# Kernel optimization log

Measured on AMD Instinct MI355X. Metric: run time of the kernel, lower is better.

Reference implementation:

```python
import jax, jax.numpy as jnp
import numpy as np

B, S = 2, 2048
HID, NH, NKV, HD = 4096, 32, 8, 128
THETA = 10000.0
WINDOW = 1024  # sliding window size


def setup_inputs() -> dict:
    key = jax.random.key(0)
    k1, k2, k3 = jax.random.split(key, 3)
    hidden_states = jax.random.normal(k1, (B, S, HID), jnp.float32)
    wqkv = jax.random.normal(k2, (HID, (NH + 2 * NKV) * HD), jnp.float32) * 0.02
    wo = jax.random.normal(k3, (NH * HD, HID), jnp.float32) * 0.02
    positions = jnp.arange(S, dtype=jnp.int32)
    return {"hidden_states": hidden_states, "wqkv": wqkv, "wo": wo, "positions": positions}


def _rope_neox(x, positions):
    # x: [B, S, h, HD]; GPT-NeoX style: rotate concatenated halves.
    half = HD // 2
    inv_freq = 1.0 / (THETA ** (jnp.arange(half, dtype=jnp.float32) / half))
    ang = positions.astype(jnp.float32)[:, None] * inv_freq  # [S, half]
    cos = jnp.cos(ang)[None, :, None, :]
    sin = jnp.sin(ang)[None, :, None, :]
    x1, x2 = jnp.split(x, 2, axis=-1)
    return jnp.concatenate([x1 * cos - x2 * sin, x2 * cos + x1 * sin], axis=-1)


def reference(hidden_states, wqkv, wo, positions):
    qkv = hidden_states @ wqkv  # [B, S, (NH+2*NKV)*HD]
    q, k, v = jnp.split(qkv, [NH * HD, NH * HD + NKV * HD], axis=-1)
    q = q.reshape(B, S, NH, HD)
    k = k.reshape(B, S, NKV, HD)
    v = v.reshape(B, S, NKV, HD)
    q = _rope_neox(q, positions)
    k = _rope_neox(k, positions)
    # GQA: each KV head serves NH // NKV query heads
    rep = NH // NKV
    k = jnp.repeat(k, rep, axis=2)  # [B, S, NH, HD]
    v = jnp.repeat(v, rep, axis=2)
    scale = HD ** -0.5
    scores = jnp.einsum('bqhd,bkhd->bhqk', q, k) * scale  # [B, NH, S, S]
    i = jnp.arange(S)[:, None]
    j = jnp.arange(S)[None, :]
    mask = (j <= i) & (i - j < WINDOW)  # causal + sliding window
    scores = jnp.where(mask[None, None], scores, jnp.float32(-1e30))
    probs = jax.nn.softmax(scores, axis=-1)
    attn = jnp.einsum('bhqk,bkhd->bqhd', probs, v).reshape(B, S, NH * HD)
    return attn @ wo  # [B, S, HID]
```

## Files before the change

kernel.cpp:

```cpp
#include <hip/hip_runtime.h>


typedef __attribute__((ext_vector_type(8))) short short8;
typedef __attribute__((ext_vector_type(4))) float f32x4;
typedef __attribute__((ext_vector_type(16))) float f32x16;
typedef __attribute__((ext_vector_type(4))) unsigned int u32x4;
typedef __attribute__((ext_vector_type(4))) unsigned short u16x4;

__device__ __forceinline__ unsigned short f2bf(float f) {
  unsigned int u = __builtin_bit_cast(unsigned int, f);
  u = u + 0x7fffu + ((u >> 16) & 1u);
  return (unsigned short)(u >> 16);
}
__device__ __forceinline__ float bf2f(unsigned short h) {
  unsigned int u = ((unsigned int)h) << 16;
  return __builtin_bit_cast(float, u);
}
__device__ __forceinline__ unsigned int cvtpk_bf16(float lo, float hi) {
  unsigned int r;
  asm("v_cvt_pk_bf16_f32 %0, %1, %2" : "=v"(r) : "v"(lo), "v"(hi));
  return r;
}

__device__ __forceinline__ void gload_lds16(const unsigned short* g, unsigned short* l) {
  __builtin_amdgcn_global_load_lds(
      (const __attribute__((address_space(1))) unsigned int*)g,
      (__attribute__((address_space(3))) unsigned int*)l, 16, 0, 0);
}

__device__ __forceinline__ void lds_barrier() {
  asm volatile("s_waitcnt lgkmcnt(0)" ::: "memory");
  __builtin_amdgcn_s_barrier();
}

#define MFMA16(A, B, C) __builtin_amdgcn_mfma_f32_16x16x32_bf16((A), (B), (C), 0, 0, 0)
#define MFMA32(A, B, C) __builtin_amdgcn_mfma_f32_32x32x16_bf16((A), (B), (C), 0, 0, 0)
#define BC8(x) __builtin_bit_cast(short8, (x))

__global__ __launch_bounds__(256) void cvt1(const float* __restrict__ hs,
                                            const float* __restrict__ wqkv,
                                            unsigned short* __restrict__ hsb,
                                            unsigned short* __restrict__ wT) {
  const int bid = blockIdx.x;
  if (bid < 24576) {
    __shared__ float t[32][33];
    const int c0 = (bid % 192) * 32, r0 = (bid / 192) * 32;
    const int tx = threadIdx.x & 31, ty = threadIdx.x >> 5;
#pragma unroll
    for (int i = 0; i < 4; ++i)
      t[ty + i * 8][tx] = wqkv[(size_t)(r0 + ty + i * 8) * 6144 + c0 + tx];
    __syncthreads();
#pragma unroll
    for (int i = 0; i < 4; ++i)
      wT[(size_t)(c0 + ty + i * 8) * 4096 + r0 + tx] = f2bf(t[tx][ty + i * 8]);
  } else {
    const int i = ((bid - 24576) * 256 + threadIdx.x) * 4;
    f32x4 v = *(const f32x4*)(hs + i);
    u16x4 o;
#pragma unroll
    for (int j = 0; j < 4; ++j) o[j] = f2bf(v[j]);
    *(u16x4*)(hsb + i) = o;
  }
}

__global__ __launch_bounds__(256) void rope_cvtwo(unsigned short* __restrict__ qkv,
                                                  const int* __restrict__ pos,
                                                  const float* __restrict__ wo,
                                                  unsigned short* __restrict__ wT) {
  const int bid = blockIdx.x;
  if (bid < 8192) {
    const int idx = bid * 256 + threadIdx.x;
    const int d = idx & 63;
    const int hh = (idx >> 6) & 7;
    const int tok = idx >> 9;
    const int s = tok & 2047;
    unsigned short* p = qkv + (size_t)tok * 6144 + 4096 + hh * 128 + d;
    const float x1 = bf2f(p[0]);
    const float x2 = bf2f(p[64]);
    const float inv = exp2f(-(float)d * 0.2076205059304601f);
    const float ang = (float)pos[s] * inv;
    const float c = cosf(ang), sn = sinf(ang);
    p[0]  = f2bf(x1 * c - x2 * sn);
    p[64] = f2bf(x2 * c + x1 * sn);
  } else {
    __shared__ float t[32][33];
    const int b2 = bid - 8192;
    const int c0 = (b2 % 128) * 32, r0 = (b2 / 128) * 32;
    const int tx = threadIdx.x & 31, ty = threadIdx.x >> 5;
#pragma unroll
    for (int i = 0; i < 4; ++i)
      t[ty + i * 8][tx] = wo[(size_t)(r0 + ty + i * 8) * 4096 + c0 + tx];
    __syncthreads();
#pragma unroll
    for (int i = 0; i < 4; ++i)
      wT[(size_t)(c0 + ty + i * 8) * 4096 + r0 + tx] = f2bf(t[tx][ty + i * 8]);
  }
}

template <int NIF, int OUTF32>
__global__ __launch_bounds__(512, 2) void gemm256(const unsigned short* __restrict__ A,
                                                  const unsigned short* __restrict__ BT,
                                                  void* __restrict__ Cout,
                                                  int M, int N, int K) {
  constexpr int BUFE = 16384 + NIF * 4096;
  constexpr int NR = NIF + 4;
  __shared__ __align__(16) unsigned short lds[2][BUFE];
  const int tid = threadIdx.x;
  const int lane = tid & 63;
  const int w = tid >> 6;
  const int wr = w >> 2;
  const int wc = w & 3;
  const int g = lane >> 4;
  const int l15 = lane & 15;

  const int nwg = gridDim.x;
  const int cpx = nwg >> 3;
  const int bid = blockIdx.x;
  const int swz = (bid & 7) * cpx + (bid >> 3);
  const int MT = M >> 8;
  const int m0 = (swz % MT) * 256;
  const int n0 = (swz / MT) * (NIF * 64);

  const int lrow = lane >> 3;
  const int lcol = ((lane & 7) ^ lrow) * 8;
  const unsigned short* Asrc = A + (size_t)(m0 + w * 8 + lrow) * K + lcol;
  const unsigned short* Bsrc = BT + (size_t)(n0 + w * 8 + lrow) * K + lcol;

  f32x4 acc[8][NIF] = {};

  auto stage = [&](int buf, int t, int r) {
    if (r < NIF) {
      const int rb = r * 64;
      gload_lds16(Bsrc + (size_t)rb * K + t * 64,
                  &lds[buf][16384 + (rb + w * 8) * 64]);
    } else {
      const int j = r - NIF;
      const int rb = (j & 1) * 128 + ((j >> 1) & 1) * 64;
      gload_lds16(Asrc + (size_t)rb * K + t * 64,
                  &lds[buf][(rb + w * 8) * 64]);
    }
  };
  auto rdA = [&](int buf, int mi, int ks) {
    const int row = wr * 128 + mi * 16 + l15;
    const int cb = (ks * 64 + g * 16) ^ ((l15 & 7) << 4);
    return *(const u32x4*)((const char*)&lds[buf][0] + row * 128 + cb);
  };
  auto rdB = [&](int buf, int ni, int ks) {
    const int row = wc * (NIF * 16) + ni * 16 + l15;
    const int cb = (ks * 64 + g * 16) ^ ((l15 & 7) << 4);
    return *(const u32x4*)((const char*)&lds[buf][0] + 32768 + row * 128 + cb);
  };

#pragma unroll
  for (int r = 0; r < NR; ++r) stage(0, 0, r);

  const int NT = K >> 6;
  for (int t = 0; t < NT; ++t) {
    const int cb_ = t & 1, nb_ = cb_ ^ 1;

    asm volatile("s_waitcnt vmcnt(0)" ::: "memory");
    __builtin_amdgcn_s_barrier();
    asm volatile("" ::: "memory");
    if (t + 1 < NT) {
#pragma unroll
      for (int r = 0; r < NR; ++r) stage(nb_, t + 1, r);
    }

    u32x4 bfr[NIF][2];
#pragma unroll
    for (int ni = 0; ni < NIF; ++ni) {
      bfr[ni][0] = rdB(cb_, ni, 0);
      bfr[ni][1] = rdB(cb_, ni, 1);
    }

    {
      u32x4 af[3][2];
#pragma unroll
      for (int mi = 0; mi < 3; ++mi) {
        af[mi][0] = rdA(cb_, mi, 0);
        af[mi][1] = rdA(cb_, mi, 1);
      }
      __builtin_amdgcn_s_setprio(1);
#pragma unroll
      for (int mi = 0; mi < 3; ++mi)
#pragma unroll
        for (int ni = 0; ni < NIF; ++ni) {
          acc[mi][ni] = MFMA16(BC8(af[mi][0]), BC8(bfr[ni][0]), acc[mi][ni]);
          acc[mi][ni] = MFMA16(BC8(af[mi][1]), BC8(bfr[ni][1]), acc[mi][ni]);
        }
      __builtin_amdgcn_s_setprio(0);
    }
    __builtin_amdgcn_s_barrier();
    {
      u32x4 af[3][2];
#pragma unroll
      for (int mi = 0; mi < 3; ++mi) {
        af[mi][0] = rdA(cb_, 3 + mi, 0);
        af[mi][1] = rdA(cb_, 3 + mi, 1);
      }
      __builtin_amdgcn_s_setprio(1);
#pragma unroll
      for (int mi = 0; mi < 3; ++mi)
#pragma unroll
        for (int ni = 0; ni < NIF; ++ni) {
          acc[3 + mi][ni] = MFMA16(BC8(af[mi][0]), BC8(bfr[ni][0]), acc[3 + mi][ni]);
          acc[3 + mi][ni] = MFMA16(BC8(af[mi][1]), BC8(bfr[ni][1]), acc[3 + mi][ni]);
        }
      __builtin_amdgcn_s_setprio(0);
    }
    __builtin_amdgcn_s_barrier();
    {
      u32x4 af[2][2];
#pragma unroll
      for (int mi = 0; mi < 2; ++mi) {
        af[mi][0] = rdA(cb_, 6 + mi, 0);
        af[mi][1] = rdA(cb_, 6 + mi, 1);
      }
      __builtin_amdgcn_s_setprio(1);
#pragma unroll
      for (int mi = 0; mi < 2; ++mi)
#pragma unroll
        for (int ni = 0; ni < NIF; ++ni) {
          acc[6 + mi][ni] = MFMA16(BC8(af[mi][0]), BC8(bfr[ni][0]), acc[6 + mi][ni]);
          acc[6 + mi][ni] = MFMA16(BC8(af[mi][1]), BC8(bfr[ni][1]), acc[6 + mi][ni]);
        }
      __builtin_amdgcn_s_setprio(0);
    }
  }

  const int crow0 = m0 + wr * 128;
  const int ccol0 = n0 + wc * (NIF * 16);
#pragma unroll
  for (int mi = 0; mi < 8; ++mi)
#pragma unroll
    for (int ni = 0; ni < NIF; ++ni)
#pragma unroll
      for (int r = 0; r < 4; ++r) {
        const size_t idx =
            (size_t)(crow0 + mi * 16 + g * 4 + r) * N + (ccol0 + ni * 16 + l15);
        if constexpr (OUTF32) ((float*)Cout)[idx] = acc[mi][ni][r];
        else ((unsigned short*)Cout)[idx] = f2bf(acc[mi][ni][r]);
      }
}

__global__ __launch_bounds__(512, 2) void attn_kernel(const unsigned short* __restrict__ qkv,
                                                      unsigned short* __restrict__ aout,
                                                      const int* __restrict__ pos) {
  __shared__ __align__(16) unsigned short smem[35840];

  const int tid = threadIdx.x;
  const int lane = tid & 63;
  const int w = tid >> 6;
  const int hi = lane >> 5;
  const int l31 = lane & 31;
  const int q0 = blockIdx.x * 256;
  const int h = blockIdx.y;
  const int b = blockIdx.z;
  const int kh = h >> 2;
  const size_t tokbase = (size_t)b * 2048;
  const int qw0 = q0 + w * 32;
  const int qg = qw0 + l31;

  short8 qf[8];
  {
    const unsigned short* qp = qkv + (tokbase + qg) * 6144 + h * 128;
#pragma unroll
    for (int ks8 = 0; ks8 < 8; ++ks8)
      qf[ks8] = BC8(*(const u32x4*)(qp + ks8 * 16 + hi * 8));
    const float fp = (float)pos[qg];
#pragma unroll
    for (int ks8 = 0; ks8 < 4; ++ks8)
#pragma unroll
      for (int j = 0; j < 8; ++j) {
        const int d = ks8 * 16 + hi * 8 + j;
        const float x1 = bf2f((unsigned short)qf[ks8][j]);
        const float x2 = bf2f((unsigned short)qf[ks8 + 4][j]);
        const float ang = fp * exp2f(-(float)d * 0.2076205059304601f);
        float c, sn;
        __sincosf(ang, &sn, &c);
        c *= 0.12751743f; sn *= 0.12751743f;
        qf[ks8][j]     = (short)f2bf(x1 * c - x2 * sn);
        qf[ks8 + 4][j] = (short)f2bf(x2 * c + x1 * sn);
      }
  }

  const int c0key = tid >> 4, c0col = tid & 15;
  const int c1key = (tid + 512) >> 4, c1col = tid & 15;

  u32x4 kreg[2], vreg[2];
  const unsigned short* kvK = qkv + tokbase * 6144 + 4096 + kh * 128;

  const int t0 = (q0 >= 1024 ? (q0 - 1023) >> 6 : 0);
  const int t1 = (q0 + 255) >> 6;

  {
    const unsigned short* kb = kvK + (size_t)(t0 * 64) * 6144;
    kreg[0] = *(const u32x4*)(kb + (size_t)c0key * 6144 + c0col * 8);
    kreg[1] = *(const u32x4*)(kb + (size_t)c1key * 6144 + c1col * 8);
    vreg[0] = *(const u32x4*)(kb + (size_t)c0key * 6144 + 1024 + c0col * 8);
    vreg[1] = *(const u32x4*)(kb + (size_t)c1key * 6144 + 1024 + c1col * 8);
  }

  float m_run = -1e30f, l_run = 0.0f;
  f32x16 o_acc[4] = {};

  for (int kt = t0; kt <= t1; ++kt) {
    const int cur = (kt - t0) & 1;
    unsigned short* kdst = &smem[(cur)*17920];
    unsigned short* vdst = kdst + 8704;

    if (kt == t0) {
      *(u32x4*)&kdst[c0key * 136 + c0col * 8] = kreg[0];
      *(u32x4*)&kdst[c1key * 136 + c1col * 8] = kreg[1];
#pragma unroll
      for (int e = 0; e < 8; ++e) {
        const int e0 = (e + c0col) & 7;
        const int e1 = (e + c1col) & 7;
        vdst[(c0col * 8 + e0) * 72 + c0key] =
            (unsigned short)(vreg[0][e0 >> 1] >> ((e0 & 1) * 16));
        vdst[(c1col * 8 + e1) * 72 + c1key] =
            (unsigned short)(vreg[1][e1 >> 1] >> ((e1 & 1) * 16));
      }
      if (kt < t1) {
        const unsigned short* kb = kvK + (size_t)((kt + 1) * 64) * 6144;
        kreg[0] = *(const u32x4*)(kb + (size_t)c0key * 6144 + c0col * 8);
        kreg[1] = *(const u32x4*)(kb + (size_t)c1key * 6144 + c1col * 8);
        vreg[0] = *(const u32x4*)(kb + (size_t)c0key * 6144 + 1024 + c0col * 8);
        vreg[1] = *(const u32x4*)(kb + (size_t)c1key * 6144 + 1024 + c1col * 8);
      }
      lds_barrier();
    }

    if (kt < t1) {
      unsigned short* kdn = &smem[(cur ^ 1) * 17920];
      unsigned short* vdn = kdn + 8704;
      *(u32x4*)&kdn[c0key * 136 + c0col * 8] = kreg[0];
      *(u32x4*)&kdn[c1key * 136 + c1col * 8] = kreg[1];
#pragma unroll
      for (int e = 0; e < 8; ++e) {
        const int e0 = (e + c0col) & 7;
        const int e1 = (e + c1col) & 7;
        vdn[(c0col * 8 + e0) * 72 + c0key] =
            (unsigned short)(vreg[0][e0 >> 1] >> ((e0 & 1) * 16));
        vdn[(c1col * 8 + e1) * 72 + c1key] =
            (unsigned short)(vreg[1][e1 >> 1] >> ((e1 & 1) * 16));
      }
      if (kt + 2 <= t1) {
        const unsigned short* kb = kvK + (size_t)((kt + 2) * 64) * 6144;
        kreg[0] = *(const u32x4*)(kb + (size_t)c0key * 6144 + c0col * 8);
        kreg[1] = *(const u32x4*)(kb + (size_t)c1key * 6144 + c1col * 8);
        vreg[0] = *(const u32x4*)(kb + (size_t)c0key * 6144 + 1024 + c0col * 8);
        vreg[1] = *(const u32x4*)(kb + (size_t)c1key * 6144 + 1024 + c1col * 8);
      }
    }

    const int ktb = kt * 64;
    if (ktb <= qw0 + 31 && ktb + 63 >= qw0 - 1023) {
      const unsigned short* kb = &smem[cur * 17920];
      const unsigned short* vb = kb + 8704;

      f32x16 s0 = {}, s1 = {};
      const int arow = l31 * 136 + hi * 8;
#pragma unroll
      for (int ks8 = 0; ks8 < 8; ++ks8) {
        u32x4 a0 = *(const u32x4*)&kb[arow + ks8 * 16];
        u32x4 a1 = *(const u32x4*)&kb[arow + 32 * 136 + ks8 * 16];
        s0 = MFMA32(BC8(a0), qf[ks8], s0);
        s1 = MFMA32(BC8(a1), qf[ks8], s1);
      }

      float pv[32];
      const bool need_mask = !(ktb + 63 <= qw0 && ktb >= qw0 - 992);
      if (need_mask) {
#pragma unroll
        for (int r = 0; r < 16; ++r) {
          const int key0 = ktb + ((r & 3) + 8 * (r >> 2) + 4 * hi);
          const int key1 = key0 + 32;
          pv[r]      = (key0 <= qg && qg - key0 < 1024) ? s0[r] : -1e30f;
          pv[16 + r] = (key1 <= qg && qg - key1 < 1024) ? s1[r] : -1e30f;
        }
      } else {
#pragma unroll
        for (int r = 0; r < 16; ++r) {
          pv[r] = s0[r];
          pv[16 + r] = s1[r];
        }
      }

      float mx[16];
#pragma unroll
      for (int i = 0; i < 16; ++i) mx[i] = fmaxf(pv[i], pv[i + 16]);
#pragma unroll
      for (int i = 0; i < 8; ++i) mx[i] = fmaxf(mx[i], mx[i + 8]);
#pragma unroll
      for (int i = 0; i < 4; ++i) mx[i] = fmaxf(mx[i], mx[i + 4]);
      float tm = fmaxf(fmaxf(mx[0], mx[1]), fmaxf(mx[2], mx[3]));
      tm = fmaxf(tm, __shfl_xor(tm, 32, 64));
      if (__any(tm > m_run + 11.5415603f)) {
        const float mn = fmaxf(fmaxf(m_run, tm), -1e20f);
        const float scl = exp2f(m_run - mn);
#pragma unroll
        for (int d = 0; d < 4; ++d) o_acc[d] *= scl;
        l_run *= scl;
        m_run = mn;
      }
#pragma unroll
      for (int i = 0; i < 32; ++i) pv[i] = exp2f(pv[i] - m_run);
      float sm[16];
#pragma unroll
      for (int i = 0; i < 16; ++i) sm[i] = pv[i] + pv[i + 16];
#pragma unroll
      for (int i = 0; i < 8; ++i) sm[i] = sm[i] + sm[i + 8];
#pragma unroll
      for (int i = 0; i < 4; ++i) sm[i] = sm[i] + sm[i + 4];
      float lsum = (sm[0] + sm[1]) + (sm[2] + sm[3]);
      l_run += lsum + __shfl_xor(lsum, 32, 64);

      u32x4 paf[4];
#pragma unroll
      for (int ks = 0; ks < 4; ++ks) {
        const int base = (ks >> 1) * 16 + (ks & 1) * 8;
        auto rA = __builtin_amdgcn_permlane32_swap(
            (int)cvtpk_bf16(pv[base + 0], pv[base + 1]),
            (int)cvtpk_bf16(pv[base + 4], pv[base + 5]), false, false);
        auto rB = __builtin_amdgcn_permlane32_swap(
            (int)cvtpk_bf16(pv[base + 2], pv[base + 3]),
            (int)cvtpk_bf16(pv[base + 6], pv[base + 7]), false, false);
        paf[ks][0] = (unsigned int)rA[0];
        paf[ks][1] = (unsigned int)rB[0];
        paf[ks][2] = (unsigned int)rA[1];
        paf[ks][3] = (unsigned int)rB[1];
      }

#pragma unroll
      for (int dblk = 0; dblk < 4; ++dblk) {
        const int vrow = (dblk * 32 + l31) * 72 + hi * 8;
#pragma unroll
        for (int ks = 0; ks < 4; ++ks) {
          u32x4 vf = *(const u32x4*)&vb[vrow + ks * 16];
          o_acc[dblk] = MFMA32(BC8(vf), BC8(paf[ks]), o_acc[dblk]);
        }
      }
    }

    lds_barrier();
  }

  const float rl = 1.0f / l_run;
  unsigned short* ob = &smem[w * 4352];
#pragma unroll
  for (int dblk = 0; dblk < 4; ++dblk)
#pragma unroll
    for (int rq = 0; rq < 4; ++rq) {
      u16x4 pk;
#pragma unroll
      for (int i = 0; i < 4; ++i) pk[i] = f2bf(o_acc[dblk][rq * 4 + i] * rl);
      *(u16x4*)&ob[l31 * 136 + dblk * 32 + rq * 8 + hi * 4] = pk;
    }
  lds_barrier();

  unsigned short* gout = aout + (tokbase + q0 + w * 32) * 4096 + h * 128;
#pragma unroll
  for (int r4 = 0; r4 < 8; ++r4) {
    const int row = r4 * 4 + (lane >> 4);
    u32x4 val = *(const u32x4*)&ob[row * 136 + (lane & 15) * 8];
    *(u32x4*)(gout + (size_t)row * 4096 + (lane & 15) * 8) = val;
  }
}

extern "C" void kernel_launch(void* const* d_in, const int* in_sizes, int n_in,
                              void* d_out, int out_size, void* d_ws, size_t ws_size,
                              hipStream_t stream) {
  (void)in_sizes; (void)n_in; (void)out_size; (void)ws_size;
  const float* hs   = (const float*)d_in[0];
  const float* wqkv = (const float*)d_in[1];
  const float* wo   = (const float*)d_in[2];
  const int*   pos  = (const int*)d_in[3];
  float* out = (float*)d_out;

  char* ws = (char*)d_ws;
  unsigned short* qkvb = (unsigned short*)ws;
  unsigned short* wT   = (unsigned short*)(ws + 50331648);
  unsigned short* hsb  = (unsigned short*)(ws + 100663296);

  cvt1<<<40960, 256, 0, stream>>>(hs, wqkv, hsb, wT);
  gemm256<3, 0><<<512, 512, 0, stream>>>(hsb, wT, qkvb, 4096, 6144, 4096);
  rope_cvtwo<<<24576, 256, 0, stream>>>(qkvb, pos, wo, wT);
  attn_kernel<<<dim3(8, 32, 2), 512, 0, stream>>>(qkvb, hsb, pos);
  gemm256<4, 1><<<256, 512, 0, stream>>>(hsb, wT, out, 4096, 4096, 4096);
}
```

Baseline: 488.0 us.

## Triple-buffer A tiles in QKV GEMM to prefetch two K-steps ahead

Splits the templated GEMM into a dedicated QKV kernel that keeps A tiles in a 3-deep LDS ring and B tiles double-buffered. A is prefetched two iterations ahead, and a partial vmcnt wait replaces the full drain so global loads overlap more compute. The output-projection GEMM is specialized to fixed constants without behavioral change. LDS use rises to 3x32KB + 2x24KB per block, which may exceed the budget for two blocks per CU and lower occupancy.

```diff
diff --git a/kernel.cpp b/kernel.cpp
--- a/kernel.cpp
+++ b/kernel.cpp
@@ -97,14 +97,12 @@
   }
 }
 
-template <int NIF, int OUTF32>
-__global__ __launch_bounds__(512, 2) void gemm256(const unsigned short* __restrict__ A,
-                                                  const unsigned short* __restrict__ BT,
-                                                  void* __restrict__ Cout,
-                                                  int M, int N, int K) {
-  constexpr int BUFE = 16384 + NIF * 4096;
-  constexpr int NR = NIF + 4;
-  __shared__ __align__(16) unsigned short lds[2][BUFE];
+__global__ __launch_bounds__(512, 2) void gemm_qkv(const unsigned short* __restrict__ A,
+                                                   const unsigned short* __restrict__ BT,
+                                                   unsigned short* __restrict__ Cout,
+                                                   int M, int N, int K) {
+  __shared__ __align__(16) unsigned short aB[3][16384];
+  __shared__ __align__(16) unsigned short bB[2][12288];
   const int tid = threadIdx.x;
   const int lane = tid & 63;
   const int w = tid >> 6;
@@ -119,22 +117,170 @@
   const int swz = (bid & 7) * cpx + (bid >> 3);
   const int MT = M >> 8;
   const int m0 = (swz % MT) * 256;
-  const int n0 = (swz / MT) * (NIF * 64);
+  const int n0 = (swz / MT) * 192;
 
   const int lrow = lane >> 3;
   const int lcol = ((lane & 7) ^ lrow) * 8;
   const unsigned short* Asrc = A + (size_t)(m0 + w * 8 + lrow) * K + lcol;
   const unsigned short* Bsrc = BT + (size_t)(n0 + w * 8 + lrow) * K + lcol;
 
-  f32x4 acc[8][NIF] = {};
+  f32x4 acc[8][3] = {};
+
+  auto stageA = [&](int buf, int t) {
+#pragma unroll
+    for (int j = 0; j < 4; ++j) {
+      const int rb = (j & 1) * 128 + ((j >> 1) & 1) * 64;
+      gload_lds16(Asrc + (size_t)rb * K + t * 64, &aB[buf][(rb + w * 8) * 64]);
+    }
+  };
+  auto stageB = [&](int buf, int t) {
+#pragma unroll
+    for (int r = 0; r < 3; ++r)
+      gload_lds16(Bsrc + (size_t)(r * 64) * K + t * 64,
+                  &bB[buf][(r * 64 + w * 8) * 64]);
+  };
+  auto rdA = [&](int buf, int mi, int ks) {
+    const int row = wr * 128 + mi * 16 + l15;
+    const int cb = (ks * 64 + g * 16) ^ ((l15 & 7) << 4);
+    return *(const u32x4*)((const char*)&aB[buf][0] + row * 128 + cb);
+  };
+  auto rdB = [&](int buf, int ni, int ks) {
+    const int row = wc * 48 + ni * 16 + l15;
+    const int cb = (ks * 64 + g * 16) ^ ((l15 & 7) << 4);
+    return *(const u32x4*)((const char*)&bB[buf][0] + row * 128 + cb);
+  };
+
+  stageA(0, 0);
+  stageB(0, 0);
+  stageA(1, 1);
+
+  const int NT = K >> 6;
+  int cbA = 0;
+  for (int t = 0; t < NT; ++t) {
+    const int cbB = t & 1;
+
+    if (t + 1 < NT) {
+      asm volatile("s_waitcnt vmcnt(4)" ::: "memory");
+    } else {
+      asm volatile("s_waitcnt vmcnt(0)" ::: "memory");
+    }
+    __builtin_amdgcn_s_barrier();
+    asm volatile("" ::: "memory");
+    if (t + 1 < NT) stageB(cbB ^ 1, t + 1);
+    if (t + 2 < NT) stageA((cbA + 2) % 3, t + 2);
+
+    u32x4 bfr[3][2];
+#pragma unroll
+    for (int ni = 0; ni < 3; ++ni) {
+      bfr[ni][0] = rdB(cbB, ni, 0);
+      bfr[ni][1] = rdB(cbB, ni, 1);
+    }
+
+    {
+      u32x4 af[3][2];
+#pragma unroll
+      for (int mi = 0; mi < 3; ++mi) {
+        af[mi][0] = rdA(cbA, mi, 0);
+        af[mi][1] = rdA(cbA, mi, 1);
+      }
+      __builtin_amdgcn_s_setprio(1);
+#pragma unroll
+      for (int mi = 0; mi < 3; ++mi)
+#pragma unroll
+        for (int ni = 0; ni < 3; ++ni) {
+          acc[mi][ni] = MFMA16(BC8(af[mi][0]), BC8(bfr[ni][0]), acc[mi][ni]);
+          acc[mi][ni] = MFMA16(BC8(af[mi][1]), BC8(bfr[ni][1]), acc[mi][ni]);
+        }
+      __builtin_amdgcn_s_setprio(0);
+    }
+    __builtin_amdgcn_s_barrier();
+    {
+      u32x4 af[3][2];
+#pragma unroll
+      for (int mi = 0; mi < 3; ++mi) {
+        af[mi][0] = rdA(cbA, 3 + mi, 0);
+        af[mi][1] = rdA(cbA, 3 + mi, 1);
+      }
+      __builtin_amdgcn_s_setprio(1);
+#pragma unroll
+      for (int mi = 0; mi < 3; ++mi)
+#pragma unroll
+        for (int ni = 0; ni < 3; ++ni) {
+          acc[3 + mi][ni] = MFMA16(BC8(af[mi][0]), BC8(bfr[ni][0]), acc[3 + mi][ni]);
+          acc[3 + mi][ni] = MFMA16(BC8(af[mi][1]), BC8(bfr[ni][1]), acc[3 + mi][ni]);
+        }
+      __builtin_amdgcn_s_setprio(0);
+    }
+    __builtin_amdgcn_s_barrier();
+    {
+      u32x4 af[2][2];
+#pragma unroll
+      for (int mi = 0; mi < 2; ++mi) {
+        af[mi][0] = rdA(cbA, 6 + mi, 0);
+        af[mi][1] = rdA(cbA, 6 + mi, 1);
+      }
+      __builtin_amdgcn_s_setprio(1);
+#pragma unroll
+      for (int mi = 0; mi < 2; ++mi)
+#pragma unroll
+        for (int ni = 0; ni < 3; ++ni) {
+          acc[6 + mi][ni] = MFMA16(BC8(af[mi][0]), BC8(bfr[ni][0]), acc[6 + mi][ni]);
+          acc[6 + mi][ni] = MFMA16(BC8(af[mi][1]), BC8(bfr[ni][1]), acc[6 + mi][ni]);
+        }
+      __builtin_amdgcn_s_setprio(0);
+    }
+    cbA = (cbA + 1) % 3;
+  }
+
+  const int crow0 = m0 + wr * 128;
+  const int ccol0 = n0 + wc * 48;
+#pragma unroll
+  for (int mi = 0; mi < 8; ++mi)
+#pragma unroll
+    for (int ni = 0; ni < 3; ++ni)
+#pragma unroll
+      for (int r = 0; r < 4; ++r) {
+        const size_t idx =
+            (size_t)(crow0 + mi * 16 + g * 4 + r) * N + (ccol0 + ni * 16 + l15);
+        Cout[idx] = f2bf(acc[mi][ni][r]);
+      }
+}
+
+__global__ __launch_bounds__(512, 2) void gemm256(const unsigned short* __restrict__ A,
+                                                  const unsigned short* __restrict__ BT,
+                                                  float* __restrict__ Cout,
+                                                  int M, int N, int K) {
+  __shared__ __align__(16) unsigned short lds[2][32768];
+  const int tid = threadIdx.x;
+  const int lane = tid & 63;
+  const int w = tid >> 6;
+  const int wr = w >> 2;
+  const int wc = w & 3;
+  const int g = lane >> 4;
+  const int l15 = lane & 15;
+
+  const int nwg = gridDim.x;
+  const int cpx = nwg >> 3;
+  const int bid = blockIdx.x;
+  const int swz = (bid & 7) * cpx + (bid >> 3);
+  const int MT = M >> 8;
+  const int m0 = (swz % MT) * 256;
+  const int n0 = (swz / MT) * 256;
+
+  const int lrow = lane >> 3;
+  const int lcol = ((lane & 7) ^ lrow) * 8;
+  const unsigned short* Asrc = A + (size_t)(m0 + w * 8 + lrow) * K + lcol;
+  const unsigned short* Bsrc = BT + (size_t)(n0 + w * 8 + lrow) * K + lcol;
+
+  f32x4 acc[8][4] = {};
 
   auto stage = [&](int buf, int t, int r) {
-    if (r < NIF) {
+    if (r < 4) {
       const int rb = r * 64;
       gload_lds16(Bsrc + (size_t)rb * K + t * 64,
                   &lds[buf][16384 + (rb + w * 8) * 64]);
     } else {
-      const int j = r - NIF;
+      const int j = r - 4;
       const int rb = (j & 1) * 128 + ((j >> 1) & 1) * 64;
       gload_lds16(Asrc + (size_t)rb * K + t * 64,
                   &lds[buf][(rb + w * 8) * 64]);
@@ -146,13 +292,13 @@
     return *(const u32x4*)((const char*)&lds[buf][0] + row * 128 + cb);
   };
   auto rdB = [&](int buf, int ni, int ks) {
-    const int row = wc * (NIF * 16) + ni * 16 + l15;
+    const int row = wc * 64 + ni * 16 + l15;
     const int cb = (ks * 64 + g * 16) ^ ((l15 & 7) << 4);
     return *(const u32x4*)((const char*)&lds[buf][0] + 32768 + row * 128 + cb);
   };
 
 #pragma unroll
-  for (int r = 0; r < NR; ++r) stage(0, 0, r);
+  for (int r = 0; r < 8; ++r) stage(0, 0, r);
 
   const int NT = K >> 6;
   for (int t = 0; t < NT; ++t) {
@@ -163,12 +309,12 @@
     asm volatile("" ::: "memory");
     if (t + 1 < NT) {
 #pragma unroll
-      for (int r = 0; r < NR; ++r) stage(nb_, t + 1, r);
-    }
-
-    u32x4 bfr[NIF][2];
-#pragma unroll
-    for (int ni = 0; ni < NIF; ++ni) {
+      for (int r = 0; r < 8; ++r) stage(nb_, t + 1, r);
+    }
+
+    u32x4 bfr[4][2];
+#pragma unroll
+    for (int ni = 0; ni < 4; ++ni) {
       bfr[ni][0] = rdB(cb_, ni, 0);
       bfr[ni][1] = rdB(cb_, ni, 1);
     }
@@ -184,7 +330,7 @@
 #pragma unroll
       for (int mi = 0; mi < 3; ++mi)
 #pragma unroll
-        for (int ni = 0; ni < NIF; ++ni) {
+        for (int ni = 0; ni < 4; ++ni) {
           acc[mi][ni] = MFMA16(BC8(af[mi][0]), BC8(bfr[ni][0]), acc[mi][ni]);
           acc[mi][ni] = MFMA16(BC8(af[mi][1]), BC8(bfr[ni][1]), acc[mi][ni]);
         }
@@ -202,7 +348,7 @@
 #pragma unroll
       for (int mi = 0; mi < 3; ++mi)
 #pragma unroll
-        for (int ni = 0; ni < NIF; ++ni) {
+        for (int ni = 0; ni < 4; ++ni) {
           acc[3 + mi][ni] = MFMA16(BC8(af[mi][0]), BC8(bfr[ni][0]), acc[3 + mi][ni]);
           acc[3 + mi][ni] = MFMA16(BC8(af[mi][1]), BC8(bfr[ni][1]), acc[3 + mi][ni]);
         }
@@ -220,7 +366,7 @@
 #pragma unroll
       for (int mi = 0; mi < 2; ++mi)
 #pragma unroll
-        for (int ni = 0; ni < NIF; ++ni) {
+        for (int ni = 0; ni < 4; ++ni) {
           acc[6 + mi][ni] = MFMA16(BC8(af[mi][0]), BC8(bfr[ni][0]), acc[6 + mi][ni]);
           acc[6 + mi][ni] = MFMA16(BC8(af[mi][1]), BC8(bfr[ni][1]), acc[6 + mi][ni]);
         }
@@ -229,17 +375,16 @@
   }
 
   const int crow0 = m0 + wr * 128;
-  const int ccol0 = n0 + wc * (NIF * 16);
+  const int ccol0 = n0 + wc * 64;
 #pragma unroll
   for (int mi = 0; mi < 8; ++mi)
 #pragma unroll
-    for (int ni = 0; ni < NIF; ++ni)
+    for (int ni = 0; ni < 4; ++ni)
 #pragma unroll
       for (int r = 0; r < 4; ++r) {
         const size_t idx =
             (size_t)(crow0 + mi * 16 + g * 4 + r) * N + (ccol0 + ni * 16 + l15);
-        if constexpr (OUTF32) ((float*)Cout)[idx] = acc[mi][ni][r];
-        else ((unsigned short*)Cout)[idx] = f2bf(acc[mi][ni][r]);
+        Cout[idx] = acc[mi][ni][r];
       }
 }
 
@@ -484,8 +629,8 @@
   unsigned short* hsb  = (unsigned short*)(ws + 100663296);
 
   cvt1<<<40960, 256, 0, stream>>>(hs, wqkv, hsb, wT);
-  gemm256<3, 0><<<512, 512, 0, stream>>>(hsb, wT, qkvb, 4096, 6144, 4096);
+  gemm_qkv<<<512, 512, 0, stream>>>(hsb, wT, qkvb, 4096, 6144, 4096);
   rope_cvtwo<<<24576, 256, 0, stream>>>(qkvb, pos, wo, wT);
   attn_kernel<<<dim3(8, 32, 2), 512, 0, stream>>>(qkvb, hsb, pos);
-  gemm256<4, 1><<<256, 512, 0, stream>>>(hsb, wT, out, 4096, 4096, 4096);
-}
+  gemm256<<<256, 512, 0, stream>>>(hsb, wT, out, 4096, 4096, 4096);
+}
```

Measured after the change: 531.8 us. +9.0%, slower.
